# Performance work log

Hardware: AMD Instinct MI355X
Metric: run time of the kernel (lower is better)

## Reference

```python
import jax, jax.numpy as jnp
import numpy as np

N = 8192
D_IN = 512
D_OUT = 128
DENSITY = 0.004  # avg degree ~32
NEG_INF = -1.0e10
LEAKY_ALPHA = 0.2  # tf.nn.leaky_relu default


def setup_inputs() -> dict:
    key = jax.random.key(0)
    k_x, k_adj, k_w, k_as, k_an = jax.random.split(key, 5)
    x = jax.random.normal(k_x, (N, D_IN), dtype=jnp.float32)
    # sparse binary adjacency, materialized dense (as the module does via tf.sparse.to_dense)
    adj = (jax.random.uniform(k_adj, (N, N)) < DENSITY).astype(jnp.float32)
    adj = jnp.maximum(adj, jnp.eye(N, dtype=jnp.float32))  # self-loops so softmax rows are valid
    W = jax.random.normal(k_w, (D_IN, D_OUT), dtype=jnp.float32) * (1.0 / np.sqrt(D_IN))
    attn_self = jax.random.normal(k_as, (D_OUT, 1), dtype=jnp.float32) * 0.1
    attn_neigh = jax.random.normal(k_an, (D_OUT, 1), dtype=jnp.float32) * 0.1
    return {"x": x, "adj": adj, "W": W, "attn_self": attn_self, "attn_neigh": attn_neigh}


def reference(x, adj, W, attn_self, attn_neigh):
    # dropouts are 0.0 -> identity
    h = x @ W                                   # [N, D_OUT]
    a_s = h @ attn_self                          # [N, 1]
    a_n = h @ attn_neigh                         # [N, 1]
    e = a_s + a_n.T                              # [N, N] additive attention logits
    e = jnp.where(e >= 0, e, LEAKY_ALPHA * e)    # leaky_relu
    e = e + NEG_INF * (1.0 - adj)                # mask non-edges
    attn = jax.nn.softmax(e, axis=-1)            # row-wise softmax [N, N]
    out = attn @ h                               # [N, D_OUT]
    return jax.nn.relu(out)
```

## Files before the change

### kernel.cpp

```cpp
#include <hip/hip_runtime.h>
#include <hip/hip_bf16.h>
#include <cstdint>

#define NN 8192
#define DIN 512
#define DOUT 128
#define NEG_SLOPE 0.2f
#define MAXE 256
#define GEMM_BLOCKS 1024

typedef float fvec4 __attribute__((ext_vector_type(4)));

__device__ inline fvec4 ntload4(const float* p) {
#if __has_builtin(__builtin_nontemporal_load)
    return __builtin_nontemporal_load((const fvec4*)p);
#else
    return *(const fvec4*)p;
#endif
}

__global__ __launch_bounds__(256) void k_fused(
    const float* __restrict__ x, const float* __restrict__ W,
    const float* __restrict__ attn_self, const float* __restrict__ attn_neigh,
    const float* __restrict__ adj,
    float* __restrict__ h, float* __restrict__ a_s, float* __restrict__ a_n,
    int* __restrict__ e_cnt, int* __restrict__ e_idx) {
    __shared__ char smem_raw[16384];
    __shared__ int s_cnt;
    const int tid = threadIdx.x;
    const int bid = blockIdx.x;

    if (bid < GEMM_BLOCKS) {
        float4* xs = (float4*)smem_raw;
        const int m0 = bid * 8;
        const float4* x4 = (const float4*)(x + (size_t)m0 * DIN);
#pragma unroll
        for (int r = 0; r < 4; ++r) xs[tid + 256 * r] = x4[tid + 256 * r];
        __syncthreads();

        const int c4 = tid & 31;
        const int rg = tid >> 5;
        const float4* W4 = (const float4*)W;
        const float4* xr = xs + rg * 128;
        float4 acc = {0.f, 0.f, 0.f, 0.f};
#pragma unroll 4
        for (int k4 = 0; k4 < 128; ++k4) {
            float4 xv = xr[k4];
            float4 w0 = W4[(4 * k4 + 0) * 32 + c4];
            float4 w1 = W4[(4 * k4 + 1) * 32 + c4];
            float4 w2 = W4[(4 * k4 + 2) * 32 + c4];
            float4 w3 = W4[(4 * k4 + 3) * 32 + c4];
            acc.x += xv.x * w0.x + xv.y * w1.x + xv.z * w2.x + xv.w * w3.x;
            acc.y += xv.x * w0.y + xv.y * w1.y + xv.z * w2.y + xv.w * w3.y;
            acc.z += xv.x * w0.z + xv.y * w1.z + xv.z * w2.z + xv.w * w3.z;
            acc.w += xv.x * w0.w + xv.y * w1.w + xv.z * w2.w + xv.w * w3.w;
        }
        const int row = m0 + rg;
        ((float4*)h)[(size_t)row * 32 + c4] = acc;

        float4 as4 = ((const float4*)attn_self)[c4];
        float4 an4 = ((const float4*)attn_neigh)[c4];
        float ps = acc.x * as4.x + acc.y * as4.y + acc.z * as4.z + acc.w * as4.w;
        float pn = acc.x * an4.x + acc.y * an4.y + acc.z * an4.z + acc.w * an4.w;
#pragma unroll
        for (int off = 16; off > 0; off >>= 1) {
            ps += __shfl_xor(ps, off);
            pn += __shfl_xor(pn, off);
        }
        if (c4 == 0) { a_s[row] = ps; a_n[row] = pn; }
    } else {
        const int i = bid - GEMM_BLOCKS;
        int* s_idx = (int*)smem_raw;
        if (tid == 0) s_cnt = 0;
        __syncthreads();

        const float* arow = adj + ((size_t)i << 13);
        fvec4 v[8];
#pragma unroll
        for (int r = 0; r < 8; ++r) v[r] = ntload4(arow + 4 * (tid + 256 * r));
#pragma unroll
        for (int r = 0; r < 8; ++r) {
            int base = (tid + 256 * r) * 4;
#pragma unroll
            for (int q = 0; q < 4; ++q) {
                if (v[r][q] != 0.f) {
                    int p = atomicAdd(&s_cnt, 1);
                    if (p < MAXE) s_idx[p] = base + q;
                }
            }
        }
        __syncthreads();
        const int cnt = min(s_cnt, MAXE);
        for (int t = tid; t < cnt; t += 256) e_idx[(size_t)i * MAXE + t] = s_idx[t];
        if (tid == 0) e_cnt[i] = cnt;
    }
}

__global__ __launch_bounds__(256) void k_soft(
    const float* __restrict__ h, const float* __restrict__ a_s,
    const float* __restrict__ a_n, const int* __restrict__ e_cnt,
    const int* __restrict__ e_idx, float* __restrict__ out) {
    const int i = blockIdx.x;
    const int tid = threadIdx.x;
    __shared__ int s_idx[MAXE];
    __shared__ float s_w[MAXE];
    __shared__ float s_red[4];
    __shared__ float s_red2[4];
    __shared__ float s_acc[256];

    const int cnt = e_cnt[i];
    const float asi = a_s[i];

    float m = -1e30f;
    for (int t = tid; t < cnt; t += 256) {
        int j = e_idx[(size_t)i * MAXE + t];
        s_idx[t] = j;
        float e = asi + a_n[j];
        e = (e >= 0.f) ? e : NEG_SLOPE * e;
        s_w[t] = e;
        m = fmaxf(m, e);
    }
#pragma unroll
    for (int off = 32; off > 0; off >>= 1) m = fmaxf(m, __shfl_xor(m, off));
    if ((tid & 63) == 0) s_red[tid >> 6] = m;
    __syncthreads();
    m = fmaxf(fmaxf(s_red[0], s_red[1]), fmaxf(s_red[2], s_red[3]));

    float lsum = 0.f;
    for (int t = tid; t < cnt; t += 256) {
        float w = __expf(s_w[t] - m);
        s_w[t] = w;
        lsum += w;
    }
#pragma unroll
    for (int off = 32; off > 0; off >>= 1) lsum += __shfl_xor(lsum, off);
    if ((tid & 63) == 0) s_red2[tid >> 6] = lsum;
    __syncthreads();
    const float inv_d = 1.0f / (s_red2[0] + s_red2[1] + s_red2[2] + s_red2[3]);

    const int c = tid & 127;
    const int half = tid >> 7;
    float acc = 0.f;
    int t = half;
    for (; t + 6 < cnt; t += 8) {
        float w0 = s_w[t];     int j0 = s_idx[t];
        float w1 = s_w[t + 2]; int j1 = s_idx[t + 2];
        float w2 = s_w[t + 4]; int j2 = s_idx[t + 4];
        float w3 = s_w[t + 6]; int j3 = s_idx[t + 6];
        float h0 = h[(size_t)j0 * DOUT + c];
        float h1 = h[(size_t)j1 * DOUT + c];
        float h2 = h[(size_t)j2 * DOUT + c];
        float h3 = h[(size_t)j3 * DOUT + c];
        acc += w0 * h0 + w1 * h1 + w2 * h2 + w3 * h3;
    }
    for (; t < cnt; t += 2) acc += s_w[t] * h[(size_t)s_idx[t] * DOUT + c];

    s_acc[tid] = acc;
    __syncthreads();
    if (tid < 128) {
        float tot = (s_acc[tid] + s_acc[tid + 128]) * inv_d;
        out[(size_t)i * DOUT + tid] = fmaxf(tot, 0.f);
    }
}

extern "C" void kernel_launch(void* const* d_in, const int* in_sizes, int n_in,
                              void* d_out, int out_size, void* d_ws, size_t ws_size,
                              hipStream_t stream) {
    const float* x          = (const float*)d_in[0];
    const float* adj        = (const float*)d_in[1];
    const float* W          = (const float*)d_in[2];
    const float* attn_self  = (const float*)d_in[3];
    const float* attn_neigh = (const float*)d_in[4];
    float* out = (float*)d_out;

    float* h   = (float*)d_ws;
    float* a_s = h + (size_t)NN * DOUT;
    float* a_n = a_s + NN;
    int* e_cnt = (int*)(a_n + NN);
    int* e_idx = e_cnt + NN;

    hipLaunchKernelGGL(k_fused, dim3(GEMM_BLOCKS + NN), dim3(256), 0, stream,
                       x, W, attn_self, attn_neigh, adj, h, a_s, a_n, e_cnt, e_idx);
    hipLaunchKernelGGL(k_soft, dim3(NN), dim3(256), 0, stream,
                       h, a_s, a_n, e_cnt, e_idx, out);
}
```

Baseline: 415.4 us.

## Fuse GEMM, edge compaction and softmax aggregation into one kernel with grid barrier

Merges the two kernels into a single launch. Adjacency-scanning blocks keep their compacted neighbour list in shared memory and spin on a global done counter until every GEMM block has published h, a_s and a_n, then run the softmax aggregation themselves. This drops the e_idx/e_cnt round trip through global memory and the second kernel launch, and the output is written with nontemporal stores. It adds a memset launch and relies on the GEMM blocks (lowest block ids) being scheduled before spinning blocks fill the device, which risks deadlock or stall time if dispatch order differs.

```diff
diff --git a/kernel.cpp b/kernel.cpp
--- a/kernel.cpp
+++ b/kernel.cpp
@@ -12,26 +12,29 @@
 typedef float fvec4 __attribute__((ext_vector_type(4)));
 
 __device__ inline fvec4 ntload4(const float* p) {
-#if __has_builtin(__builtin_nontemporal_load)
     return __builtin_nontemporal_load((const fvec4*)p);
-#else
-    return *(const fvec4*)p;
-#endif
+}
+__device__ inline void ntstore(float* p, float v) {
+    __builtin_nontemporal_store(v, p);
 }
 
-__global__ __launch_bounds__(256) void k_fused(
+__global__ __launch_bounds__(256) void k_all(
     const float* __restrict__ x, const float* __restrict__ W,
     const float* __restrict__ attn_self, const float* __restrict__ attn_neigh,
     const float* __restrict__ adj,
     float* __restrict__ h, float* __restrict__ a_s, float* __restrict__ a_n,
-    int* __restrict__ e_cnt, int* __restrict__ e_idx) {
-    __shared__ char smem_raw[16384];
+    int* __restrict__ done, float* __restrict__ out) {
+    __shared__ float4 xs[8 * 128];
+    __shared__ int s_idx[MAXE];
+    __shared__ float s_w[MAXE];
+    __shared__ float s_red[4];
+    __shared__ float s_red2[4];
+    __shared__ float s_acc[256];
     __shared__ int s_cnt;
     const int tid = threadIdx.x;
     const int bid = blockIdx.x;
 
     if (bid < GEMM_BLOCKS) {
-        float4* xs = (float4*)smem_raw;
         const int m0 = bid * 8;
         const float4* x4 = (const float4*)(x + (size_t)m0 * DIN);
 #pragma unroll
@@ -68,9 +71,13 @@
             pn += __shfl_xor(pn, off);
         }
         if (c4 == 0) { a_s[row] = ps; a_n[row] = pn; }
+        __syncthreads();
+        if (tid == 0) {
+            __threadfence();
+            atomicAdd(done, 1);
+        }
     } else {
         const int i = bid - GEMM_BLOCKS;
-        int* s_idx = (int*)smem_raw;
         if (tid == 0) s_cnt = 0;
         __syncthreads();
 
@@ -89,77 +96,64 @@
                 }
             }
         }
+        if (tid == 0) {
+            while (__hip_atomic_load(done, __ATOMIC_ACQUIRE,
+                                     __HIP_MEMORY_SCOPE_AGENT) < GEMM_BLOCKS)
+                __builtin_amdgcn_s_sleep(8);
+        }
         __syncthreads();
         const int cnt = min(s_cnt, MAXE);
-        for (int t = tid; t < cnt; t += 256) e_idx[(size_t)i * MAXE + t] = s_idx[t];
-        if (tid == 0) e_cnt[i] = cnt;
-    }
-}
+        const float asi = a_s[i];
 
-__global__ __launch_bounds__(256) void k_soft(
-    const float* __restrict__ h, const float* __restrict__ a_s,
-    const float* __restrict__ a_n, const int* __restrict__ e_cnt,
-    const int* __restrict__ e_idx, float* __restrict__ out) {
-    const int i = blockIdx.x;
-    const int tid = threadIdx.x;
-    __shared__ int s_idx[MAXE];
-    __shared__ float s_w[MAXE];
-    __shared__ float s_red[4];
-    __shared__ float s_red2[4];
-    __shared__ float s_acc[256];
+        float m = -1e30f;
+        for (int t = tid; t < cnt; t += 256) {
+            int j = s_idx[t];
+            float e = asi + a_n[j];
+            e = (e >= 0.f) ? e : NEG_SLOPE * e;
+            s_w[t] = e;
+            m = fmaxf(m, e);
+        }
+#pragma unroll
+        for (int off = 32; off > 0; off >>= 1) m = fmaxf(m, __shfl_xor(m, off));
+        if ((tid & 63) == 0) s_red[tid >> 6] = m;
+        __syncthreads();
+        m = fmaxf(fmaxf(s_red[0], s_red[1]), fmaxf(s_red[2], s_red[3]));
 
-    const int cnt = e_cnt[i];
-    const float asi = a_s[i];
+        float lsum = 0.f;
+        for (int t = tid; t < cnt; t += 256) {
+            float w = __expf(s_w[t] - m);
+            s_w[t] = w;
+            lsum += w;
+        }
+#pragma unroll
+        for (int off = 32; off > 0; off >>= 1) lsum += __shfl_xor(lsum, off);
+        if ((tid & 63) == 0) s_red2[tid >> 6] = lsum;
+        __syncthreads();
+        const float inv_d = 1.0f / (s_red2[0] + s_red2[1] + s_red2[2] + s_red2[3]);
 
-    float m = -1e30f;
-    for (int t = tid; t < cnt; t += 256) {
-        int j = e_idx[(size_t)i * MAXE + t];
-        s_idx[t] = j;
-        float e = asi + a_n[j];
-        e = (e >= 0.f) ? e : NEG_SLOPE * e;
-        s_w[t] = e;
-        m = fmaxf(m, e);
-    }
-#pragma unroll
-    for (int off = 32; off > 0; off >>= 1) m = fmaxf(m, __shfl_xor(m, off));
-    if ((tid & 63) == 0) s_red[tid >> 6] = m;
-    __syncthreads();
-    m = fmaxf(fmaxf(s_red[0], s_red[1]), fmaxf(s_red[2], s_red[3]));
+        const int c = tid & 127;
+        const int half = tid >> 7;
+        float acc = 0.f;
+        int t = half;
+        for (; t + 6 < cnt; t += 8) {
+            float w0 = s_w[t];     int j0 = s_idx[t];
+            float w1 = s_w[t + 2]; int j1 = s_idx[t + 2];
+            float w2 = s_w[t + 4]; int j2 = s_idx[t + 4];
+            float w3 = s_w[t + 6]; int j3 = s_idx[t + 6];
+            float h0 = h[(size_t)j0 * DOUT + c];
+            float h1 = h[(size_t)j1 * DOUT + c];
+            float h2 = h[(size_t)j2 * DOUT + c];
+            float h3 = h[(size_t)j3 * DOUT + c];
+            acc += w0 * h0 + w1 * h1 + w2 * h2 + w3 * h3;
+        }
+        for (; t < cnt; t += 2) acc += s_w[t] * h[(size_t)s_idx[t] * DOUT + c];
 
-    float lsum = 0.f;
-    for (int t = tid; t < cnt; t += 256) {
-        float w = __expf(s_w[t] - m);
-        s_w[t] = w;
-        lsum += w;
-    }
-#pragma unroll
-    for (int off = 32; off > 0; off >>= 1) lsum += __shfl_xor(lsum, off);
-    if ((tid & 63) == 0) s_red2[tid >> 6] = lsum;
-    __syncthreads();
-    const float inv_d = 1.0f / (s_red2[0] + s_red2[1] + s_red2[2] + s_red2[3]);
-
-    const int c = tid & 127;
-    const int half = tid >> 7;
-    float acc = 0.f;
-    int t = half;
-    for (; t + 6 < cnt; t += 8) {
-        float w0 = s_w[t];     int j0 = s_idx[t];
-        float w1 = s_w[t + 2]; int j1 = s_idx[t + 2];
-        float w2 = s_w[t + 4]; int j2 = s_idx[t + 4];
-        float w3 = s_w[t + 6]; int j3 = s_idx[t + 6];
-        float h0 = h[(size_t)j0 * DOUT + c];
-        float h1 = h[(size_t)j1 * DOUT + c];
-        float h2 = h[(size_t)j2 * DOUT + c];
-        float h3 = h[(size_t)j3 * DOUT + c];
-        acc += w0 * h0 + w1 * h1 + w2 * h2 + w3 * h3;
-    }
-    for (; t < cnt; t += 2) acc += s_w[t] * h[(size_t)s_idx[t] * DOUT + c];
-
-    s_acc[tid] = acc;
-    __syncthreads();
-    if (tid < 128) {
-        float tot = (s_acc[tid] + s_acc[tid + 128]) * inv_d;
-        out[(size_t)i * DOUT + tid] = fmaxf(tot, 0.f);
+        s_acc[tid] = acc;
+        __syncthreads();
+        if (tid < 128) {
+            float tot = (s_acc[tid] + s_acc[tid + 128]) * inv_d;
+            ntstore(out + (size_t)i * DOUT + tid, fmaxf(tot, 0.f));
+        }
     }
 }
 
@@ -176,11 +170,9 @@
     float* h   = (float*)d_ws;
     float* a_s = h + (size_t)NN * DOUT;
     float* a_n = a_s + NN;
-    int* e_cnt = (int*)(a_n + NN);
-    int* e_idx = e_cnt + NN;
+    int* done  = (int*)(a_n + NN);
 
-    hipLaunchKernelGGL(k_fused, dim3(GEMM_BLOCKS + NN), dim3(256), 0, stream,
-                       x, W, attn_self, attn_neigh, adj, h, a_s, a_n, e_cnt, e_idx);
-    hipLaunchKernelGGL(k_soft, dim3(NN), dim3(256), 0, stream,
-                       h, a_s, a_n, e_cnt, e_idx, out);
+    hipMemsetAsync(done, 0, sizeof(int), stream);
+    hipLaunchKernelGGL(k_all, dim3(GEMM_BLOCKS + NN), dim3(256), 0, stream,
+                       x, W, attn_self, attn_neigh, adj, h, a_s, a_n, done, out);
 }
```

Result: slower. 1.081 ms (+160.2%).
